# Performance work log

Hardware: AMD Instinct MI355X
Metric: run time of the kernel (lower is better)

Reference implementation:

```python
import jax, jax.numpy as jnp
import numpy as np

D = 768
H = 12
HD = 64
S = 77
FF = 3072
EPS = 1e-5


def _layernorm(x, w, b):
    mu = jnp.mean(x, axis=-1, keepdims=True)
    var = jnp.mean(jnp.square(x - mu), axis=-1, keepdims=True)
    return (x - mu) * jax.lax.rsqrt(var + EPS) * w + b


def setup_inputs() -> dict:
    key = jax.random.key(0)
    ks = jax.random.split(key, 18)
    s = 1.0 / np.sqrt(D)
    sf = 1.0 / np.sqrt(FF)
    return {
        "x": jax.random.normal(ks[0], (512, S, D), dtype=jnp.float32),
        "ln1_w": jnp.ones((D,), jnp.float32),
        "ln1_b": jnp.zeros((D,), jnp.float32),
        "qw": jax.random.uniform(ks[1], (D, D), jnp.float32, -s, s),
        "qb": jax.random.uniform(ks[2], (D,), jnp.float32, -s, s),
        "kw": jax.random.uniform(ks[3], (D, D), jnp.float32, -s, s),
        "kb": jax.random.uniform(ks[4], (D,), jnp.float32, -s, s),
        "vw": jax.random.uniform(ks[5], (D, D), jnp.float32, -s, s),
        "vb": jax.random.uniform(ks[6], (D,), jnp.float32, -s, s),
        "ow": jax.random.uniform(ks[7], (D, D), jnp.float32, -s, s),
        "ob": jax.random.uniform(ks[8], (D,), jnp.float32, -s, s),
        "ln2_w": jnp.ones((D,), jnp.float32),
        "ln2_b": jnp.zeros((D,), jnp.float32),
        "fc1_w": jax.random.uniform(ks[9], (FF, D), jnp.float32, -s, s),
        "fc1_b": jax.random.uniform(ks[10], (FF,), jnp.float32, -s, s),
        "fc2_w": jax.random.uniform(ks[11], (D, FF), jnp.float32, -sf, sf),
        "fc2_b": jax.random.uniform(ks[12], (D,), jnp.float32, -sf, sf),
    }


def reference(x, ln1_w, ln1_b, qw, qb, kw, kb, vw, vb, ow, ob,
              ln2_w, ln2_b, fc1_w, fc1_b, fc2_w, fc2_b):
    B = x.shape[0]
    # --- attention block ---
    h = _layernorm(x, ln1_w, ln1_b)
    q = (h @ qw.T + qb) * 0.125
    k = h @ kw.T + kb
    v = h @ vw.T + vb
    # [B, S, H, HD] -> [B, H, S, HD]
    q = q.reshape(B, S, H, HD).transpose(0, 2, 1, 3)
    k = k.reshape(B, S, H, HD).transpose(0, 2, 1, 3)
    v = v.reshape(B, S, H, HD).transpose(0, 2, 1, 3)
    scores = jnp.einsum('bhqd,bhkd->bhqk', q, k)  # [B,H,S,S]
    # causal additive mask: -inf strictly above diagonal
    mask = jnp.triu(jnp.full((S, S), -jnp.inf, dtype=scores.dtype), 1)
    scores = scores + mask
    attn = jax.nn.softmax(scores, axis=-1)
    ctx = jnp.einsum('bhqk,bhkd->bhqd', attn, v)  # [B,H,S,HD]
    ctx = ctx.transpose(0, 2, 1, 3).reshape(B, S, D)
    x = x + (ctx @ ow.T + ob)
    # --- MLP block with QuickGELU ---
    res = x
    h2 = _layernorm(x, ln2_w, ln2_b) @ fc1_w.T + fc1_b
    h2 = h2 * jax.nn.sigmoid(h2 * 1.702)
    return res + (h2 @ fc2_w.T + fc2_b)
```

## Files before the change

kernel.cpp:

```cpp
#include <hip/hip_runtime.h>

typedef unsigned short u16;
typedef __bf16 v8bf __attribute__((ext_vector_type(8)));
typedef unsigned short u16x8 __attribute__((ext_vector_type(8)));
typedef float v4f __attribute__((ext_vector_type(4)));

#define DEV __device__ __forceinline__

constexpr int M_TOK = 512 * 77;

DEV u16 f2bf(float f) {
  union { float f; unsigned int u; } v; v.f = f;
  unsigned int r = v.u + 0x7fffu + ((v.u >> 16) & 1u);
  return (u16)(r >> 16);
}

DEV void gload16(const void* g, void* l) {
  __builtin_amdgcn_global_load_lds((const __attribute__((address_space(1))) void*)g,
                                   (__attribute__((address_space(3))) void*)l, 16, 0, 0);
}

DEV v4f MF(v8bf a, v8bf b, v4f c) {
  return __builtin_amdgcn_mfma_f32_16x16x32_bf16(a, b, c, 0, 0, 0);
}

__global__ void cvt4_k(const float* __restrict__ src, u16* __restrict__ dst, int n4, float scale) {
  int i = blockIdx.x * blockDim.x + threadIdx.x;
  if (i >= n4) return;
  const float4 v = ((const float4*)src)[i];
  ushort4 o;
  o.x = f2bf(v.x * scale); o.y = f2bf(v.y * scale);
  o.z = f2bf(v.z * scale); o.w = f2bf(v.w * scale);
  ((ushort4*)dst)[i] = o;
}

__global__ void qkvb_k(const float* __restrict__ qb, const float* __restrict__ kb,
                       const float* __restrict__ vb, float* __restrict__ dst) {
  int i = blockIdx.x * 256 + threadIdx.x;
  if (i >= 2304) return;
  dst[i] = (i < 768) ? qb[i] * 0.125f : (i < 1536 ? kb[i - 768] : vb[i - 1536]);
}

__global__ __launch_bounds__(256) void ln_k(const float* __restrict__ x, const float* __restrict__ w,
                                            const float* __restrict__ bvec, u16* __restrict__ out, int nrows) {
  const int lane = threadIdx.x & 63;
  const int row = blockIdx.x * 4 + (threadIdx.x >> 6);
  if (row >= nrows) return;
  const float4* xr = (const float4*)(x + (size_t)row * 768);
  float4 v[3];
  float sum = 0.f, sq = 0.f;
#pragma unroll
  for (int t = 0; t < 3; ++t) {
    v[t] = xr[lane + 64 * t];
    sum += v[t].x + v[t].y + v[t].z + v[t].w;
    sq  += v[t].x * v[t].x + v[t].y * v[t].y + v[t].z * v[t].z + v[t].w * v[t].w;
  }
#pragma unroll
  for (int o = 1; o < 64; o <<= 1) { sum += __shfl_xor(sum, o, 64); sq += __shfl_xor(sq, o, 64); }
  const float mean = sum * (1.f / 768.f);
  const float inv = rsqrtf(sq * (1.f / 768.f) - mean * mean + 1e-5f);
  u16* orow = out + (size_t)row * 768;
#pragma unroll
  for (int t = 0; t < 3; ++t) {
    const int c = 4 * (lane + 64 * t);
    ushort4 o4;
    o4.x = f2bf((v[t].x - mean) * inv * w[c + 0] + bvec[c + 0]);
    o4.y = f2bf((v[t].y - mean) * inv * w[c + 1] + bvec[c + 1]);
    o4.z = f2bf((v[t].z - mean) * inv * w[c + 2] + bvec[c + 2]);
    o4.w = f2bf((v[t].w - mean) * inv * w[c + 3] + bvec[c + 3]);
    *(ushort4*)(orow + c) = o4;
  }
}

template <int OUTF32, int ACT, int RES>
__global__ __launch_bounds__(512, 2) void gemmP_k(
    const u16* __restrict__ A, const u16* __restrict__ Bw,
    const float* __restrict__ bias, const float* __restrict__ res,
    void* __restrict__ out, int M, int N, int K, int nbx) {
  __shared__ u16 lds[73728];
  const int tid = threadIdx.x;
  const int lane = tid & 63;
  const int wv = tid >> 6;
  const int wr = wv >> 2, wc = wv & 3;

  const int nwg = gridDim.x;
  const int q8 = nwg >> 3, r8 = nwg & 7;
  const int xcd = blockIdx.x & 7, cidx = blockIdx.x >> 3;
  const int wg = (xcd < r8 ? xcd * (q8 + 1) : r8 * (q8 + 1) + (xcd - r8) * q8) + cidx;
  const int m0 = (wg / nbx) * 128;
  const int n0 = (wg % nbx) * 256;

  const int frow = lane & 15, fq = lane >> 4;
  const int e = frow & 7;
  const int aB = (wr * 64 + frow) * 64 + ((fq ^ e) * 8);
  const int bB = 8192 + (wc * 64 + frow) * 64 + ((fq ^ e) * 8);

  const int srow = tid >> 3;
  const int cOff = ((tid & 7) ^ (srow & 7)) * 8;
  const u16* pA = A + (size_t)(m0 + srow) * K + cOff;
  const u16* pB = Bw + (size_t)(n0 + srow) * K + cOff;
  const size_t K64 = (size_t)K * 64;
  const int ldsW = wv * 512;

#define LD(IDX) (*(const v8bf*)&lds[IDX])
#define BAR() asm volatile("s_barrier" ::: "memory")
#define STAGE(t, s) do {                                                        \
    const int sb_ = (s) * 24576;                                                \
    gload16(pA + 0 * K64 + (size_t)(t) * 64, &lds[sb_ + 0 * 4096 + ldsW]);      \
    gload16(pA + 1 * K64 + (size_t)(t) * 64, &lds[sb_ + 1 * 4096 + ldsW]);      \
    gload16(pB + 0 * K64 + (size_t)(t) * 64, &lds[sb_ + 8192 + 0 * 4096 + ldsW]); \
    gload16(pB + 1 * K64 + (size_t)(t) * 64, &lds[sb_ + 8192 + 1 * 4096 + ldsW]); \
    gload16(pB + 2 * K64 + (size_t)(t) * 64, &lds[sb_ + 8192 + 2 * 4096 + ldsW]); \
    gload16(pB + 3 * K64 + (size_t)(t) * 64, &lds[sb_ + 8192 + 3 * 4096 + ldsW]); \
  } while (0)
#define READSET(S, rb) do {                                                     \
    _Pragma("unroll")                                                           \
    for (int i_ = 0; i_ < 4; ++i_) {                                            \
      Af[S][i_]     = LD((rb) + aB + i_ * 1024);                                \
      Af[S][4 + i_] = LD(((rb) + aB + i_ * 1024) ^ 32);                         \
      Bf[S][i_]     = LD((rb) + bB + i_ * 1024);                                \
      Bf[S][4 + i_] = LD(((rb) + bB + i_ * 1024) ^ 32);                         \
    }                                                                           \
  } while (0)
#define MFMA32(S) do {                                                          \
    _Pragma("unroll")                                                           \
    for (int i_ = 0; i_ < 4; ++i_)                                              \
      _Pragma("unroll")                                                         \
      for (int j_ = 0; j_ < 4; ++j_)                                            \
        acc[i_][j_] = MF(Af[S][i_], Bf[S][j_], acc[i_][j_]);                    \
    _Pragma("unroll")                                                           \
    for (int i_ = 0; i_ < 4; ++i_)                                              \
      _Pragma("unroll")                                                         \
      for (int j_ = 0; j_ < 4; ++j_)                                            \
        acc[i_][j_] = MF(Af[S][4 + i_], Bf[S][4 + j_], acc[i_][j_]);            \
  } while (0)
#define BODY(kt, S, NS) do {                                                    \
    const int stg_ = (kt) + 3;                                                  \
    if (stg_ < NT) STAGE(stg_, stg_ % 3);                                       \
    if ((kt) + 1 < NT) { READSET(NS, (((kt) + 1) % 3) * 24576); }               \
    __builtin_amdgcn_s_setprio(1);                                              \
    MFMA32(S);                                                                  \
    __builtin_amdgcn_s_setprio(0);                                              \
    asm volatile("s_waitcnt lgkmcnt(0)" ::: "memory");                          \
    __builtin_amdgcn_sched_barrier(0);                                          \
    if (stg_ < NT) { asm volatile("s_waitcnt vmcnt(6)" ::: "memory"); }         \
    else           { asm volatile("s_waitcnt vmcnt(0)" ::: "memory"); }         \
    __builtin_amdgcn_sched_barrier(0);                                          \
    BAR();                                                                      \
  } while (0)

  v8bf Af[2][8], Bf[2][8];
  v4f acc[4][4];
#pragma unroll
  for (int i = 0; i < 4; ++i)
#pragma unroll
    for (int j = 0; j < 4; ++j) acc[i][j] = (v4f){0.f, 0.f, 0.f, 0.f};

  const int NT = K >> 6;

  STAGE(0, 0); STAGE(1, 1); STAGE(2, 2);
  asm volatile("s_waitcnt vmcnt(6)" ::: "memory");
  BAR();
  READSET(0, 0);

  for (int kt2 = 0; kt2 < (NT >> 1); ++kt2) {
    const int kt = kt2 * 2;
    BODY(kt, 0, 1);
    BODY(kt + 1, 1, 0);
  }
#undef BODY
#undef MFMA32
#undef READSET
#undef STAGE
#undef LD
#undef BAR

#pragma unroll
  for (int i = 0; i < 4; ++i) {
    const int rowb = m0 + wr * 64 + i * 16 + fq * 4;
#pragma unroll
    for (int j = 0; j < 4; ++j) {
      const int col = n0 + wc * 64 + j * 16 + frow;
      const float bv = bias[col];
#pragma unroll
      for (int rr = 0; rr < 4; ++rr) {
        float v = acc[i][j][rr] + bv;
        if (ACT) v = v * (1.f / (1.f + __expf(-1.702f * v)));
        const size_t off = (size_t)(rowb + rr) * N + col;
        if (RES) v += res[off];
        if (OUTF32) ((float*)out)[off] = v;
        else ((u16*)out)[off] = f2bf(v);
      }
    }
  }
}

__global__ __launch_bounds__(256) void attn_k(const u16* __restrict__ qkv, u16* __restrict__ ctx) {
  __shared__ u16 sQK[10240];
  __shared__ u16 sVt[64 * 120];
  __shared__ float sS[80][81];
  const int tid = threadIdx.x;
  const int lane = tid & 63;
  const int wv = tid >> 6;
  const int b = blockIdx.x / 12;
  const int h = blockIdx.x % 12;
  u16* sQ = sQK;
  u16* sK = sQK + 5120;
  u16* sP = sQK;

  for (int i = tid; i < 10240 + 64 * 120; i += 256) {
    if (i < 10240) sQK[i] = 0; else sVt[i - 10240] = 0;
  }
  __syncthreads();

  const size_t tokBase = (size_t)(b * 77) * 2304 + h * 64;
  for (int c = tid; c < 77 * 8; c += 256) {
    const int row = c >> 3, k8 = (c & 7) * 8;
    const size_t src = tokBase + (size_t)row * 2304 + k8;
    *(u16x8*)&sQ[row * 64 + k8] = *(const u16x8*)&qkv[src];
    *(u16x8*)&sK[row * 64 + k8] = *(const u16x8*)&qkv[src + 768];
    u16x8 v = *(const u16x8*)&qkv[src + 1536];
#pragma unroll
    for (int j = 0; j < 8; ++j) sVt[(k8 + j) * 120 + row] = v[j];
  }
  __syncthreads();

  const int frow = lane & 15, fk = (lane >> 4) * 8;
  for (int t = wv; t < 25; t += 4) {
    const int it = t / 5, jt = t % 5;
    v4f acc = {0.f, 0.f, 0.f, 0.f};
#pragma unroll
    for (int kk = 0; kk < 2; ++kk) {
      v8bf a = *(const v8bf*)&sQ[(it * 16 + frow) * 64 + kk * 32 + fk];
      v8bf bb = *(const v8bf*)&sK[(jt * 16 + frow) * 64 + kk * 32 + fk];
      acc = MF(a, bb, acc);
    }
    const int col = jt * 16 + frow;
#pragma unroll
    for (int r = 0; r < 4; ++r) {
      const int row = it * 16 + (lane >> 4) * 4 + r;
      sS[row][col] = (col > row) ? -1e30f : acc[r];
    }
  }
  __syncthreads();

  if (tid < 80) {
    const int row = tid;
    float mx = -1e30f;
    for (int c2 = 0; c2 < 80; ++c2) mx = fmaxf(mx, sS[row][c2]);
    float sum = 0.f;
    for (int c2 = 0; c2 < 80; ++c2) { float e = __expf(sS[row][c2] - mx); sum += e; sS[row][c2] = e; }
    const float inv = 1.f / sum;
    for (int c2 = 0; c2 < 80; ++c2) sP[row * 96 + c2] = f2bf(sS[row][c2] * inv);
    for (int c2 = 80; c2 < 96; ++c2) sP[row * 96 + c2] = 0;
  }
  __syncthreads();

  const size_t outBase = (size_t)(b * 77) * 768 + h * 64;
  for (int t = wv; t < 20; t += 4) {
    const int it = t / 4, jt = t % 4;
    v4f acc = {0.f, 0.f, 0.f, 0.f};
#pragma unroll
    for (int kk = 0; kk < 3; ++kk) {
      v8bf a = *(const v8bf*)&sP[(it * 16 + frow) * 96 + kk * 32 + fk];
      v8bf bb = *(const v8bf*)&sVt[(jt * 16 + frow) * 120 + kk * 32 + fk];
      acc = MF(a, bb, acc);
    }
    const int col = jt * 16 + frow;
#pragma unroll
    for (int r = 0; r < 4; ++r) {
      const int row = it * 16 + (lane >> 4) * 4 + r;
      if (row < 77) ctx[outBase + (size_t)row * 768 + col] = f2bf(acc[r]);
    }
  }
}

extern "C" void kernel_launch(void* const* d_in, const int* in_sizes, int n_in,
                              void* d_out, int out_size, void* d_ws, size_t ws_size,
                              hipStream_t stream) {
  const float* x    = (const float*)d_in[0];
  const float* ln1w = (const float*)d_in[1];
  const float* ln1b = (const float*)d_in[2];
  const float* qw   = (const float*)d_in[3];
  const float* qb   = (const float*)d_in[4];
  const float* kw   = (const float*)d_in[5];
  const float* kb   = (const float*)d_in[6];
  const float* vw   = (const float*)d_in[7];
  const float* vb   = (const float*)d_in[8];
  const float* ow   = (const float*)d_in[9];
  const float* ob   = (const float*)d_in[10];
  const float* ln2w = (const float*)d_in[11];
  const float* ln2b = (const float*)d_in[12];
  const float* f1wf = (const float*)d_in[13];
  const float* f1b  = (const float*)d_in[14];
  const float* f2wf = (const float*)d_in[15];
  const float* f2b  = (const float*)d_in[16];
  float* outp = (float*)d_out;

  char* p = (char*)d_ws;
  auto alloc = [&](size_t bytes) { char* r = p; p += (bytes + 255) & ~(size_t)255; return r; };
  u16* wqkv = (u16*)alloc((size_t)2304 * 768 * 2);
  u16* owb  = (u16*)alloc((size_t)768 * 768 * 2);
  u16* f1w  = (u16*)alloc((size_t)3072 * 768 * 2);
  u16* f2w  = (u16*)alloc((size_t)768 * 3072 * 2);
  float* qkvb = (float*)alloc(2304 * 4);
  u16* bufA = (u16*)alloc((size_t)M_TOK * 768 * 2);
  u16* bufB = (u16*)alloc((size_t)M_TOK * 3072 * 2);

  cvt4_k<<<576, 256, 0, stream>>>(qw, wqkv, 147456, 0.125f);
  cvt4_k<<<576, 256, 0, stream>>>(kw, wqkv + 589824, 147456, 1.f);
  cvt4_k<<<576, 256, 0, stream>>>(vw, wqkv + 1179648, 147456, 1.f);
  cvt4_k<<<576, 256, 0, stream>>>(ow, owb, 147456, 1.f);
  cvt4_k<<<2304, 256, 0, stream>>>(f1wf, f1w, 589824, 1.f);
  cvt4_k<<<2304, 256, 0, stream>>>(f2wf, f2w, 589824, 1.f);
  qkvb_k<<<9, 256, 0, stream>>>(qb, kb, vb, qkvb);

  ln_k<<<M_TOK / 4, 256, 0, stream>>>(x, ln1w, ln1b, bufA, M_TOK);
  gemmP_k<0, 0, 0><<<308 * 9, 512, 0, stream>>>(bufA, wqkv, qkvb, nullptr, bufB, M_TOK, 2304, 768, 9);
  attn_k<<<512 * 12, 256, 0, stream>>>(bufB, bufA);
  gemmP_k<1, 0, 1><<<308 * 3, 512, 0, stream>>>(bufA, owb, ob, x, outp, M_TOK, 768, 768, 3);
  ln_k<<<M_TOK / 4, 256, 0, stream>>>(outp, ln2w, ln2b, bufA, M_TOK);
  gemmP_k<0, 1, 0><<<308 * 12, 512, 0, stream>>>(bufA, f1w, f1b, nullptr, bufB, M_TOK, 3072, 768, 12);
  gemmP_k<1, 0, 1><<<308 * 3, 512, 0, stream>>>(bufB, f2w, f2b, outp, outp, M_TOK, 768, 3072, 3);
}
```

Measured before the change: 1.034 ms.

## Shrink GEMM tiles to 128x128 with 4 waves and double-buffered LDS

Replaces the 128x256, 8-wave GEMM with a 128x128 tile on 256 threads (2x2 waves). The pipeline drops from triple to double buffering, with a full vmcnt(0) wait each iteration, and LDS use falls from 144KB to 64KB per block. The aim is higher occupancy and twice as many workgroups across the CUs. In exchange, each tile reuses fewer B bytes, global traffic per FLOP goes up, and the full load wait each iteration makes memory latency harder to hide.

```diff
diff --git a/kernel.cpp b/kernel.cpp
--- a/kernel.cpp
+++ b/kernel.cpp
@@ -73,22 +73,22 @@
 }
 
 template <int OUTF32, int ACT, int RES>
-__global__ __launch_bounds__(512, 2) void gemmP_k(
+__global__ __launch_bounds__(256, 2) void gemmR_k(
     const u16* __restrict__ A, const u16* __restrict__ Bw,
     const float* __restrict__ bias, const float* __restrict__ res,
     void* __restrict__ out, int M, int N, int K, int nbx) {
-  __shared__ u16 lds[73728];
+  __shared__ u16 lds[32768];
   const int tid = threadIdx.x;
   const int lane = tid & 63;
   const int wv = tid >> 6;
-  const int wr = wv >> 2, wc = wv & 3;
+  const int wr = wv >> 1, wc = wv & 1;
 
   const int nwg = gridDim.x;
   const int q8 = nwg >> 3, r8 = nwg & 7;
   const int xcd = blockIdx.x & 7, cidx = blockIdx.x >> 3;
   const int wg = (xcd < r8 ? xcd * (q8 + 1) : r8 * (q8 + 1) + (xcd - r8) * q8) + cidx;
   const int m0 = (wg / nbx) * 128;
-  const int n0 = (wg % nbx) * 256;
+  const int n0 = (wg % nbx) * 128;
 
   const int frow = lane & 15, fq = lane >> 4;
   const int e = frow & 7;
@@ -99,54 +99,51 @@
   const int cOff = ((tid & 7) ^ (srow & 7)) * 8;
   const u16* pA = A + (size_t)(m0 + srow) * K + cOff;
   const u16* pB = Bw + (size_t)(n0 + srow) * K + cOff;
-  const size_t K64 = (size_t)K * 64;
+  const size_t K32 = (size_t)K * 32;
   const int ldsW = wv * 512;
 
 #define LD(IDX) (*(const v8bf*)&lds[IDX])
 #define BAR() asm volatile("s_barrier" ::: "memory")
-#define STAGE(t, s) do {                                                        \
-    const int sb_ = (s) * 24576;                                                \
-    gload16(pA + 0 * K64 + (size_t)(t) * 64, &lds[sb_ + 0 * 4096 + ldsW]);      \
-    gload16(pA + 1 * K64 + (size_t)(t) * 64, &lds[sb_ + 1 * 4096 + ldsW]);      \
-    gload16(pB + 0 * K64 + (size_t)(t) * 64, &lds[sb_ + 8192 + 0 * 4096 + ldsW]); \
-    gload16(pB + 1 * K64 + (size_t)(t) * 64, &lds[sb_ + 8192 + 1 * 4096 + ldsW]); \
-    gload16(pB + 2 * K64 + (size_t)(t) * 64, &lds[sb_ + 8192 + 2 * 4096 + ldsW]); \
-    gload16(pB + 3 * K64 + (size_t)(t) * 64, &lds[sb_ + 8192 + 3 * 4096 + ldsW]); \
+#define STAGE(t, s) do { const int sb_ = (s) << 14;                                   \
+    gload16(pA + 0 * K32 + (size_t)(t) * 64, &lds[sb_ + 0 * 2048 + ldsW]);            \
+    gload16(pA + 1 * K32 + (size_t)(t) * 64, &lds[sb_ + 1 * 2048 + ldsW]);            \
+    gload16(pA + 2 * K32 + (size_t)(t) * 64, &lds[sb_ + 2 * 2048 + ldsW]);            \
+    gload16(pA + 3 * K32 + (size_t)(t) * 64, &lds[sb_ + 3 * 2048 + ldsW]);            \
+    gload16(pB + 0 * K32 + (size_t)(t) * 64, &lds[sb_ + 8192 + 0 * 2048 + ldsW]);     \
+    gload16(pB + 1 * K32 + (size_t)(t) * 64, &lds[sb_ + 8192 + 1 * 2048 + ldsW]);     \
+    gload16(pB + 2 * K32 + (size_t)(t) * 64, &lds[sb_ + 8192 + 2 * 2048 + ldsW]);     \
+    gload16(pB + 3 * K32 + (size_t)(t) * 64, &lds[sb_ + 8192 + 3 * 2048 + ldsW]);     \
   } while (0)
-#define READSET(S, rb) do {                                                     \
-    _Pragma("unroll")                                                           \
-    for (int i_ = 0; i_ < 4; ++i_) {                                            \
-      Af[S][i_]     = LD((rb) + aB + i_ * 1024);                                \
-      Af[S][4 + i_] = LD(((rb) + aB + i_ * 1024) ^ 32);                         \
-      Bf[S][i_]     = LD((rb) + bB + i_ * 1024);                                \
-      Bf[S][4 + i_] = LD(((rb) + bB + i_ * 1024) ^ 32);                         \
-    }                                                                           \
+#define READSET(S, sb) do {                                                           \
+    _Pragma("unroll")                                                                 \
+    for (int i_ = 0; i_ < 4; ++i_) {                                                  \
+      Af[S][i_]     = LD((sb) + aB + i_ * 1024);                                      \
+      Af[S][4 + i_] = LD(((sb) + aB + i_ * 1024) ^ 32);                               \
+      Bf[S][i_]     = LD((sb) + bB + i_ * 1024);                                      \
+      Bf[S][4 + i_] = LD(((sb) + bB + i_ * 1024) ^ 32);                               \
+    }                                                                                 \
   } while (0)
-#define MFMA32(S) do {                                                          \
-    _Pragma("unroll")                                                           \
-    for (int i_ = 0; i_ < 4; ++i_)                                              \
-      _Pragma("unroll")                                                         \
-      for (int j_ = 0; j_ < 4; ++j_)                                            \
-        acc[i_][j_] = MF(Af[S][i_], Bf[S][j_], acc[i_][j_]);                    \
-    _Pragma("unroll")                                                           \
-    for (int i_ = 0; i_ < 4; ++i_)                                              \
-      _Pragma("unroll")                                                         \
-      for (int j_ = 0; j_ < 4; ++j_)                                            \
-        acc[i_][j_] = MF(Af[S][4 + i_], Bf[S][4 + j_], acc[i_][j_]);            \
+#define MFMA32(S) do {                                                                \
+    _Pragma("unroll")                                                                 \
+    for (int i_ = 0; i_ < 4; ++i_)                                                    \
+      _Pragma("unroll")                                                               \
+      for (int j_ = 0; j_ < 4; ++j_)                                                  \
+        acc[i_][j_] = MF(Af[S][i_], Bf[S][j_], acc[i_][j_]);                          \
+    _Pragma("unroll")                                                                 \
+    for (int i_ = 0; i_ < 4; ++i_)                                                    \
+      _Pragma("unroll")                                                               \
+      for (int j_ = 0; j_ < 4; ++j_)                                                  \
+        acc[i_][j_] = MF(Af[S][4 + i_], Bf[S][4 + j_], acc[i_][j_]);                  \
   } while (0)
-#define BODY(kt, S, NS) do {                                                    \
-    const int stg_ = (kt) + 3;                                                  \
-    if (stg_ < NT) STAGE(stg_, stg_ % 3);                                       \
-    if ((kt) + 1 < NT) { READSET(NS, (((kt) + 1) % 3) * 24576); }               \
-    __builtin_amdgcn_s_setprio(1);                                              \
-    MFMA32(S);                                                                  \
-    __builtin_amdgcn_s_setprio(0);                                              \
-    asm volatile("s_waitcnt lgkmcnt(0)" ::: "memory");                          \
-    __builtin_amdgcn_sched_barrier(0);                                          \
-    if (stg_ < NT) { asm volatile("s_waitcnt vmcnt(6)" ::: "memory"); }         \
-    else           { asm volatile("s_waitcnt vmcnt(0)" ::: "memory"); }         \
-    __builtin_amdgcn_sched_barrier(0);                                          \
-    BAR();                                                                      \
+#define BODY(kt, CUR, NXT) do {                                                       \
+    if ((kt) + 2 < NT) STAGE((kt) + 2, (kt) & 1);                                     \
+    if ((kt) + 1 < NT) READSET(NXT, (((kt) + 1) & 1) << 14);                          \
+    __builtin_amdgcn_s_setprio(1);                                                    \
+    MFMA32(CUR);                                                                      \
+    __builtin_amdgcn_s_setprio(0);                                                    \
+    asm volatile("s_waitcnt lgkmcnt(0)" ::: "memory");                                \
+    asm volatile("s_waitcnt vmcnt(0)" ::: "memory");                                  \
+    BAR();                                                                            \
   } while (0)
 
   v8bf Af[2][8], Bf[2][8];
@@ -158,15 +155,16 @@
 
   const int NT = K >> 6;
 
-  STAGE(0, 0); STAGE(1, 1); STAGE(2, 2);
-  asm volatile("s_waitcnt vmcnt(6)" ::: "memory");
+  STAGE(0, 0); STAGE(1, 1);
+  asm volatile("s_waitcnt vmcnt(0)" ::: "memory");
   BAR();
   READSET(0, 0);
+  asm volatile("s_waitcnt lgkmcnt(0)" ::: "memory");
+  BAR();
 
   for (int kt2 = 0; kt2 < (NT >> 1); ++kt2) {
-    const int kt = kt2 * 2;
-    BODY(kt, 0, 1);
-    BODY(kt + 1, 1, 0);
+    BODY(2 * kt2, 0, 1);
+    BODY(2 * kt2 + 1, 1, 0);
   }
 #undef BODY
 #undef MFMA32
@@ -249,7 +247,7 @@
     float mx = -1e30f;
     for (int c2 = 0; c2 < 80; ++c2) mx = fmaxf(mx, sS[row][c2]);
     float sum = 0.f;
-    for (int c2 = 0; c2 < 80; ++c2) { float e = __expf(sS[row][c2] - mx); sum += e; sS[row][c2] = e; }
+    for (int c2 = 0; c2 < 80; ++c2) { float e2 = __expf(sS[row][c2] - mx); sum += e2; sS[row][c2] = e2; }
     const float inv = 1.f / sum;
     for (int c2 = 0; c2 < 80; ++c2) sP[row * 96 + c2] = f2bf(sS[row][c2] * inv);
     for (int c2 = 80; c2 < 96; ++c2) sP[row * 96 + c2] = 0;
@@ -316,10 +314,10 @@
   qkvb_k<<<9, 256, 0, stream>>>(qb, kb, vb, qkvb);
 
   ln_k<<<M_TOK / 4, 256, 0, stream>>>(x, ln1w, ln1b, bufA, M_TOK);
-  gemmP_k<0, 0, 0><<<308 * 9, 512, 0, stream>>>(bufA, wqkv, qkvb, nullptr, bufB, M_TOK, 2304, 768, 9);
+  gemmR_k<0, 0, 0><<<308 * 18, 256, 0, stream>>>(bufA, wqkv, qkvb, nullptr, bufB, M_TOK, 2304, 768, 18);
   attn_k<<<512 * 12, 256, 0, stream>>>(bufB, bufA);
-  gemmP_k<1, 0, 1><<<308 * 3, 512, 0, stream>>>(bufA, owb, ob, x, outp, M_TOK, 768, 768, 3);
+  gemmR_k<1, 0, 1><<<308 * 6, 256, 0, stream>>>(bufA, owb, ob, x, outp, M_TOK, 768, 768, 6);
   ln_k<<<M_TOK / 4, 256, 0, stream>>>(outp, ln2w, ln2b, bufA, M_TOK);
-  gemmP_k<0, 1, 0><<<308 * 12, 512, 0, stream>>>(bufA, f1w, f1b, nullptr, bufB, M_TOK, 3072, 768, 12);
-  gemmP_k<1, 0, 1><<<308 * 3, 512, 0, stream>>>(bufB, f2w, f2b, outp, outp, M_TOK, 768, 3072, 3);
-}
+  gemmR_k<0, 1, 0><<<308 * 24, 256, 0, stream>>>(bufA, f1w, f1b, nullptr, bufB, M_TOK, 3072, 768, 24);
+  gemmR_k<1, 0, 1><<<308 * 6, 256, 0, stream>>>(bufB, f2w, f2b, outp, outp, M_TOK, 768, 3072, 6);
+}
```

Result: faster. 974.8 us (-5.7%).
